# Kernel optimization log

Hardware: AMD Instinct MI355X
Metric: run time of the kernel (lower is better)

## Reference

```python
import jax, jax.numpy as jnp
import numpy as np

NUM_ITERS = 5
MIN_SCALE = 0.5
MAX_SCALE = 2.0
EPS = 1e-8


def setup_inputs() -> dict:
    key = jax.random.key(0)
    k1, k2 = jax.random.split(key)
    B, N, M = 16, 4096, 4096
    source = jax.random.normal(k1, (B, N, 3), dtype=jnp.float32)
    target = jax.random.normal(k2, (B, M, 3), dtype=jnp.float32)
    return {"source": source, "target": target}


def _sq_cdist(a, b):
    # squared euclidean distance matrix (B,N,M) via quadratic expansion
    a2 = jnp.sum(a * a, axis=-1)[:, :, None]
    b2 = jnp.sum(b * b, axis=-1)[:, None, :]
    ab = jnp.einsum('bnd,bmd->bnm', a, b)
    return jnp.maximum(a2 + b2 - 2.0 * ab, 0.0)


def _umeyama(source, target_corr):
    # optimal similarity transform (R, t, scale), Umeyama
    B = source.shape[0]
    mu_src = jnp.mean(source, axis=1, keepdims=True)       # (B,1,3)
    mu_tgt = jnp.mean(target_corr, axis=1, keepdims=True)  # (B,1,3)
    src_c = source - mu_src
    tgt_c = target_corr - mu_tgt
    H = jnp.einsum('bnd,bne->bde', src_c, tgt_c)           # (B,3,3)
    U, S, Vh = jnp.linalg.svd(H)
    V = jnp.swapaxes(Vh, 1, 2)
    det_UV = jnp.linalg.det(jnp.einsum('bij,bkj->bik', V, U))  # det(V U^T)
    d_diag = jnp.concatenate(
        [jnp.ones((B, 2), dtype=source.dtype), det_UV[:, None]], axis=1)  # (B,3)
    # R = V @ diag(d) @ U^T
    R = jnp.einsum('bij,bj,bkj->bik', V, d_diag, U)
    var_src = jnp.sum(src_c * src_c, axis=(1, 2))          # (B,)
    trace_S = jnp.sum(S * d_diag, axis=1)                  # (B,)
    scale = (trace_S / (var_src + EPS))[:, None, None]
    scale = jnp.clip(scale, MIN_SCALE, MAX_SCALE)
    t = mu_tgt - scale * jnp.einsum('bnd,bed->bne', mu_src, R)
    return R, t, scale


def reference(source, target):
    # ICP iterations (no-grad in original -> stop_gradient on final transform)
    src_current = source
    for _ in range(NUM_ITERS):
        dist = _sq_cdist(src_current, target)              # (B,N,M)
        min_idx = jnp.argmin(dist, axis=2)                 # (B,N)
        tgt_corr = jnp.take_along_axis(target, min_idx[:, :, None], axis=1)
        R, t, scale = _umeyama(source, tgt_corr)
        src_current = scale * jnp.einsum('bnd,bed->bne', source, R) + t
    R = jax.lax.stop_gradient(R)
    t = jax.lax.stop_gradient(t)
    scale = jax.lax.stop_gradient(scale)
    aligned_source = scale * jnp.einsum('bnd,bed->bne', source, R) + t
    final_dist = _sq_cdist(aligned_source, target)
    min_src2tgt = jnp.min(final_dist, axis=2)
    min_tgt2src = jnp.min(final_dist, axis=1)
    chamfer = jnp.mean(min_src2tgt, axis=1) + jnp.mean(min_tgt2src, axis=1)
    return jnp.mean(chamfer), aligned_source
```

## Files before the change

kernel.cpp:

```cpp
#include <hip/hip_runtime.h>
#include <math.h>

#define BLOCK 256
#define NB    16
#define NN_   4096
#define MM_   4096
#define NITER 5
#define P     4
#define SCH   4
#define KCH   16
#define TCH   256
#define KCHF  8
#define TCHF  512

#define OFF_STATS 0
#define OFF_T     64
#define OFF_CH    320
#define OFF_PART  336
#define OFF_ND    1280
#define OFF_FA    1280
#define OFF_FB    525568

typedef __attribute__((ext_vector_type(2))) float f32x2;

__device__ __forceinline__ f32x2 pk_fma(f32x2 a, f32x2 b, f32x2 c) {
  f32x2 d;
  asm("v_pk_fma_f32 %0, %1, %2, %3" : "=v"(d) : "v"(a), "v"(b), "v"(c));
  return d;
}

__global__ __launch_bounds__(BLOCK) void icp_init(const float* __restrict__ src,
                                                  float* __restrict__ ws) {
  int b = blockIdx.x, tid = threadIdx.x;
  const float* sb = src + (size_t)b * NN_ * 3;
  float sx = 0.f, sy = 0.f, sz = 0.f, ss = 0.f;
  for (int n = tid; n < NN_; n += BLOCK) {
    float x = sb[3*n], y = sb[3*n+1], z = sb[3*n+2];
    sx += x; sy += y; sz += z;
    ss += fmaf(x, x, fmaf(y, y, z*z));
  }
  __shared__ float red[16];
  for (int m = 32; m; m >>= 1) {
    sx += __shfl_xor(sx, m); sy += __shfl_xor(sy, m);
    sz += __shfl_xor(sz, m); ss += __shfl_xor(ss, m);
  }
  int wave = tid >> 6;
  if ((tid & 63) == 0) {
    red[wave*4+0] = sx; red[wave*4+1] = sy; red[wave*4+2] = sz; red[wave*4+3] = ss;
  }
  __syncthreads();
  if (tid == 0) {
    for (int w = 1; w < 4; ++w) {
      sx += red[w*4+0]; sy += red[w*4+1]; sz += red[w*4+2]; ss += red[w*4+3];
    }
    float* st = ws + OFF_STATS + b*4;
    st[0] = sx; st[1] = sy; st[2] = sz; st[3] = ss;
    float* T = ws + OFF_T + b*16;
    T[0]=1.f; T[1]=0.f; T[2]=0.f;
    T[3]=0.f; T[4]=1.f; T[5]=0.f;
    T[6]=0.f; T[7]=0.f; T[8]=1.f;
    T[9]=0.f; T[10]=0.f; T[11]=0.f; T[12]=1.f;
  }
}

__global__ __launch_bounds__(BLOCK) void icp_nn1(const float* __restrict__ src,
                                                 const float* __restrict__ tgt,
                                                 float* __restrict__ ws) {
  __shared__ float tx_[TCH], ty_[TCH], tz_[TCH], tw_[TCH];
  int b = blockIdx.z, kc = blockIdx.y, tid = threadIdx.x;
  int n0 = blockIdx.x * (BLOCK * P) + tid;
  const float* T = ws + OFF_T + b*16;
  float sc = T[12];
  f32x2 nxp[P], nyp[P], nzp[P];
#pragma unroll
  for (int k = 0; k < P; ++k) {
    const float* sp = src + ((size_t)b * NN_ + n0 + k*BLOCK) * 3;
    float sx = sp[0], sy = sp[1], sz = sp[2];
    float px = fmaf(sc, fmaf(T[0], sx, fmaf(T[1], sy, T[2]*sz)), T[9]);
    float py = fmaf(sc, fmaf(T[3], sx, fmaf(T[4], sy, T[5]*sz)), T[10]);
    float pz = fmaf(sc, fmaf(T[6], sx, fmaf(T[7], sy, T[8]*sz)), T[11]);
    nxp[k].x = nxp[k].y = -2.f*px;
    nyp[k].x = nyp[k].y = -2.f*py;
    nzp[k].x = nzp[k].y = -2.f*pz;
  }
  {
    int j = tid;
    const float* tp = tgt + ((size_t)b * MM_ + kc * TCH + j) * 3;
    float tx = tp[0], ty = tp[1], tz = tp[2];
    tx_[j] = tx; ty_[j] = ty; tz_[j] = tz;
    tw_[j] = fmaf(tx, tx, fmaf(ty, ty, tz*tz));
  }
  __syncthreads();

  int jbase = kc * TCH;
  float best[P];
#pragma unroll
  for (int k = 0; k < P; ++k) best[k] = INFINITY;
#pragma unroll 4
  for (int j = 0; j < TCH; j += 2) {
    f32x2 TX = *(const f32x2*)&tx_[j];
    f32x2 TY = *(const f32x2*)&ty_[j];
    f32x2 TZ = *(const f32x2*)&tz_[j];
    f32x2 TW = *(const f32x2*)&tw_[j];
#pragma unroll
    for (int k = 0; k < P; ++k) {
      f32x2 v = pk_fma(nxp[k], TX, pk_fma(nyp[k], TY, pk_fma(nzp[k], TZ, TW)));
      float p0 = __uint_as_float((__float_as_uint(v.x) & 0xFFFFF000u) |
                                 ((unsigned)(jbase + j) & 0xFFFu));
      float p1 = __uint_as_float((__float_as_uint(v.y) & 0xFFFFF000u) |
                                 ((unsigned)(jbase + j + 1) & 0xFFFu));
      best[k] = fminf(fminf(p0, p1), best[k]);
    }
  }
#pragma unroll
  for (int k = 0; k < P; ++k)
    ws[OFF_ND + (size_t)(b*KCH + kc)*NN_ + n0 + k*BLOCK] = best[k];
}

__global__ __launch_bounds__(BLOCK) void icp_nn2(const float* __restrict__ src,
                                                 const float* __restrict__ tgt,
                                                 float* __restrict__ ws) {
  __shared__ float red[4*12];
  int b = blockIdx.y, c4 = blockIdx.x, tid = threadIdx.x;
  float acc[12];
#pragma unroll
  for (int c = 0; c < 12; ++c) acc[c] = 0.f;
  for (int k = 0; k < P; ++k) {
    int n = c4 * (BLOCK*P) + tid + k*BLOCK;
    float bd = INFINITY;
#pragma unroll
    for (int c = 0; c < KCH; ++c)
      bd = fminf(bd, ws[OFF_ND + (size_t)(b*KCH + c)*NN_ + n]);
    int bi = (int)(__float_as_uint(bd) & 4095u);
    const float* tp = tgt + ((size_t)b * MM_ + bi) * 3;
    const float* sp = src + ((size_t)b * NN_ + n) * 3;
    float tx = tp[0], ty = tp[1], tz = tp[2];
    float sx = sp[0], sy = sp[1], sz = sp[2];
    acc[0] += tx; acc[1] += ty; acc[2] += tz;
    acc[3] += sx*tx; acc[4] += sx*ty; acc[5] += sx*tz;
    acc[6] += sy*tx; acc[7] += sy*ty; acc[8] += sy*tz;
    acc[9] += sz*tx; acc[10] += sz*ty; acc[11] += sz*tz;
  }
#pragma unroll
  for (int c = 0; c < 12; ++c)
    for (int m = 32; m; m >>= 1) acc[c] += __shfl_xor(acc[c], m);
  int wave = tid >> 6;
  if ((tid & 63) == 0) {
#pragma unroll
    for (int c = 0; c < 12; ++c) red[wave*12 + c] = acc[c];
  }
  __syncthreads();
  if (tid < 12) {
    float s = red[tid] + red[12+tid] + red[24+tid] + red[36+tid];
    ws[OFF_PART + (b*SCH + c4)*12 + tid] = s;
  }
}

__global__ __launch_bounds__(64) void icp_umeyama(float* __restrict__ ws) {
  int b = blockIdx.x, tid = threadIdx.x;
  __shared__ double sums[12];
  if (tid < 12) {
    double s = 0.0;
    for (int j = 0; j < SCH; ++j)
      s += (double)ws[OFF_PART + (b*SCH + j)*12 + tid];
    sums[tid] = s;
  }
  __syncthreads();
  if (tid != 0) return;

  const float* st = ws + OFF_STATS + b*4;
  const double N = (double)NN_;
  double mus[3] = {st[0]/N, st[1]/N, st[2]/N};
  double var_src = (double)st[3] - N*(mus[0]*mus[0] + mus[1]*mus[1] + mus[2]*mus[2]);
  double mut[3] = {sums[0]/N, sums[1]/N, sums[2]/N};
  double H[3][3];
  for (int d = 0; d < 3; ++d)
    for (int e = 0; e < 3; ++e)
      H[d][e] = sums[3 + 3*d + e] - N*mus[d]*mut[e];

  double A[3][3];
  for (int i = 0; i < 3; ++i)
    for (int j = 0; j < 3; ++j)
      A[i][j] = H[0][i]*H[0][j] + H[1][i]*H[1][j] + H[2][i]*H[2][j];
  double V[3][3] = {{1,0,0},{0,1,0},{0,0,1}};
  const int PP[3] = {0,0,1}, QQ[3] = {1,2,2};
  for (int sweep = 0; sweep < 14; ++sweep) {
    for (int r = 0; r < 3; ++r) {
      int p = PP[r], q = QQ[r];
      double apq = A[p][q];
      if (fabs(apq) < 1e-300) continue;
      double tau = (A[q][q] - A[p][p]) / (2.0*apq);
      double tt = (tau >= 0.0 ? 1.0 : -1.0) / (fabs(tau) + sqrt(1.0 + tau*tau));
      double c = 1.0 / sqrt(1.0 + tt*tt), s = tt*c;
      for (int k = 0; k < 3; ++k) { double akp=A[k][p], akq=A[k][q];
        A[k][p]=c*akp - s*akq; A[k][q]=s*akp + c*akq; }
      for (int k = 0; k < 3; ++k) { double apk=A[p][k], aqk=A[q][k];
        A[p][k]=c*apk - s*aqk; A[q][k]=s*apk + c*aqk; }
      for (int k = 0; k < 3; ++k) { double vkp=V[k][p], vkq=V[k][q];
        V[k][p]=c*vkp - s*vkq; V[k][q]=s*vkp + c*vkq; }
    }
  }
  double lam[3] = {A[0][0], A[1][1], A[2][2]};
  int o[3] = {0,1,2};
  if (lam[o[1]] > lam[o[0]]) { int t_=o[0]; o[0]=o[1]; o[1]=t_; }
  if (lam[o[2]] > lam[o[0]]) { int t_=o[0]; o[0]=o[2]; o[2]=t_; }
  if (lam[o[2]] > lam[o[1]]) { int t_=o[1]; o[1]=o[2]; o[2]=t_; }
  double v0[3] = {V[0][o[0]], V[1][o[0]], V[2][o[0]]};
  double v1[3] = {V[0][o[1]], V[1][o[1]], V[2][o[1]]};
  double v2[3] = {V[0][o[2]], V[1][o[2]], V[2][o[2]]};

  double hv0[3], hv1[3], hv2[3];
  for (int d = 0; d < 3; ++d) {
    hv0[d] = H[d][0]*v0[0] + H[d][1]*v0[1] + H[d][2]*v0[2];
    hv1[d] = H[d][0]*v1[0] + H[d][1]*v1[1] + H[d][2]*v1[2];
    hv2[d] = H[d][0]*v2[0] + H[d][1]*v2[1] + H[d][2]*v2[2];
  }
  double S0 = sqrt(hv0[0]*hv0[0] + hv0[1]*hv0[1] + hv0[2]*hv0[2]);
  double u0[3];
  double inv0 = (S0 > 1e-30) ? 1.0/S0 : 0.0;
  u0[0]=hv0[0]*inv0; u0[1]=hv0[1]*inv0; u0[2]=hv0[2]*inv0;
  if (S0 <= 1e-30) { u0[0]=1.0; u0[1]=0.0; u0[2]=0.0; }
  double S1 = sqrt(hv1[0]*hv1[0] + hv1[1]*hv1[1] + hv1[2]*hv1[2]);
  double d01 = u0[0]*hv1[0] + u0[1]*hv1[1] + u0[2]*hv1[2];
  double w1[3] = {hv1[0]-d01*u0[0], hv1[1]-d01*u0[1], hv1[2]-d01*u0[2]};
  double n1 = sqrt(w1[0]*w1[0] + w1[1]*w1[1] + w1[2]*w1[2]);
  double u1[3];
  if (n1 > 1e-30) { u1[0]=w1[0]/n1; u1[1]=w1[1]/n1; u1[2]=w1[2]/n1; }
  else {
    double ax = fabs(u0[0]);
    double t0[3] = { ax < 0.9 ? 1.0 : 0.0, ax < 0.9 ? 0.0 : 1.0, 0.0 };
    u1[0] = u0[1]*t0[2]-u0[2]*t0[1];
    u1[1] = u0[2]*t0[0]-u0[0]*t0[2];
    u1[2] = u0[0]*t0[1]-u0[1]*t0[0];
    double nn = sqrt(u1[0]*u1[0]+u1[1]*u1[1]+u1[2]*u1[2]);
    u1[0]/=nn; u1[1]/=nn; u1[2]/=nn;
  }
  double u2[3] = {u0[1]*u1[2]-u0[2]*u1[1],
                  u0[2]*u1[0]-u0[0]*u1[2],
                  u0[0]*u1[1]-u0[1]*u1[0]};
  double s2p = u2[0]*hv2[0] + u2[1]*hv2[1] + u2[2]*hv2[2];
  double dV = v0[0]*(v1[1]*v2[2]-v1[2]*v2[1])
            - v0[1]*(v1[0]*v2[2]-v1[2]*v2[0])
            + v0[2]*(v1[0]*v2[1]-v1[1]*v2[0]);
  dV = (dV >= 0.0) ? 1.0 : -1.0;
  double traceS = S0 + S1 + dV * s2p;

  double R[3][3];
  for (int i = 0; i < 3; ++i)
    for (int k = 0; k < 3; ++k)
      R[i][k] = v0[i]*u0[k] + v1[i]*u1[k] + dV*v2[i]*u2[k];

  double scale = traceS / (var_src + 1e-8);
  scale = fmin(fmax(scale, 0.5), 2.0);
  double tv[3];
  for (int e = 0; e < 3; ++e)
    tv[e] = mut[e] - scale*(R[e][0]*mus[0] + R[e][1]*mus[1] + R[e][2]*mus[2]);

  float* T = ws + OFF_T + b*16;
  for (int e = 0; e < 3; ++e)
    for (int d = 0; d < 3; ++d)
      T[3*e + d] = (float)R[e][d];
  T[9]  = (float)tv[0]; T[10] = (float)tv[1]; T[11] = (float)tv[2];
  T[12] = (float)scale;
}

__global__ __launch_bounds__(BLOCK) void icp_final(const float* __restrict__ src,
                                                   const float* __restrict__ tgt,
                                                   float* __restrict__ out,
                                                   float* __restrict__ ws) {
  __shared__ float tx_[TCHF], ty_[TCHF], tz_[TCHF], tw_[TCHF];
  int b = blockIdx.z, yk = blockIdx.y, tid = threadIdx.x;
  int dir = yk >> 3, kc = yk & 7;
  const float* T = ws + OFF_T + b*16;
  float sc = T[12];
  int n0 = blockIdx.x * (BLOCK * P) + tid;
  f32x2 nxp[P], nyp[P], nzp[P];
  float pp[P];

  if (dir == 0) {
#pragma unroll
    for (int k = 0; k < P; ++k) {
      const float* sp = src + ((size_t)b * NN_ + n0 + k*BLOCK) * 3;
      float sx = sp[0], sy = sp[1], sz = sp[2];
      float px = fmaf(sc, fmaf(T[0], sx, fmaf(T[1], sy, T[2]*sz)), T[9]);
      float py = fmaf(sc, fmaf(T[3], sx, fmaf(T[4], sy, T[5]*sz)), T[10]);
      float pz = fmaf(sc, fmaf(T[6], sx, fmaf(T[7], sy, T[8]*sz)), T[11]);
      if (kc == 0) {
        float* op = out + 1 + ((size_t)b * NN_ + n0 + k*BLOCK) * 3;
        op[0] = px; op[1] = py; op[2] = pz;
      }
      pp[k] = fmaf(px, px, fmaf(py, py, pz*pz));
      nxp[k].x = nxp[k].y = -2.f*px;
      nyp[k].x = nyp[k].y = -2.f*py;
      nzp[k].x = nzp[k].y = -2.f*pz;
    }
    const float* tb = tgt + ((size_t)b * MM_ + kc * TCHF) * 3;
    for (int j = tid; j < TCHF; j += BLOCK) {
      float tx = tb[3*j], ty = tb[3*j+1], tz = tb[3*j+2];
      tx_[j] = tx; ty_[j] = ty; tz_[j] = tz;
      tw_[j] = fmaf(tx, tx, fmaf(ty, ty, tz*tz));
    }
  } else {
#pragma unroll
    for (int k = 0; k < P; ++k) {
      const float* qp = tgt + ((size_t)b * MM_ + n0 + k*BLOCK) * 3;
      float qx = qp[0], qy = qp[1], qz = qp[2];
      pp[k] = fmaf(qx, qx, fmaf(qy, qy, qz*qz));
      nxp[k].x = nxp[k].y = -2.f*qx;
      nyp[k].x = nyp[k].y = -2.f*qy;
      nzp[k].x = nzp[k].y = -2.f*qz;
    }
    const float* sb = src + ((size_t)b * NN_ + kc * TCHF) * 3;
    for (int j = tid; j < TCHF; j += BLOCK) {
      float sx = sb[3*j], sy = sb[3*j+1], sz = sb[3*j+2];
      float ax = fmaf(sc, fmaf(T[0], sx, fmaf(T[1], sy, T[2]*sz)), T[9]);
      float ay = fmaf(sc, fmaf(T[3], sx, fmaf(T[4], sy, T[5]*sz)), T[10]);
      float az = fmaf(sc, fmaf(T[6], sx, fmaf(T[7], sy, T[8]*sz)), T[11]);
      tx_[j] = ax; ty_[j] = ay; tz_[j] = az;
      tw_[j] = fmaf(ax, ax, fmaf(ay, ay, az*az));
    }
  }
  __syncthreads();

  float best[P];
#pragma unroll
  for (int k = 0; k < P; ++k) best[k] = INFINITY;
#pragma unroll 4
  for (int j = 0; j < TCHF; j += 2) {
    f32x2 TX = *(const f32x2*)&tx_[j];
    f32x2 TY = *(const f32x2*)&ty_[j];
    f32x2 TZ = *(const f32x2*)&tz_[j];
    f32x2 TW = *(const f32x2*)&tw_[j];
#pragma unroll
    for (int k = 0; k < P; ++k) {
      f32x2 v = pk_fma(nxp[k], TX, pk_fma(nyp[k], TY, pk_fma(nzp[k], TZ, TW)));
      best[k] = fminf(fminf(v.x, v.y), best[k]);
    }
  }
  float* dst = ws + (dir ? OFF_FB : OFF_FA);
#pragma unroll
  for (int k = 0; k < P; ++k)
    dst[(size_t)(b*KCHF + kc)*NN_ + n0 + k*BLOCK] = best[k] + pp[k];
}

__global__ __launch_bounds__(BLOCK) void icp_fcomb(float* __restrict__ ws) {
  __shared__ float red[4*2];
  int b = blockIdx.x, tid = threadIdx.x;
  float sa = 0.f, sb = 0.f;
  for (int g = 0; g < NN_/BLOCK; ++g) {
    int n = g*BLOCK + tid;
    float m1 = INFINITY, m2 = INFINITY;
#pragma unroll
    for (int c = 0; c < KCHF; ++c) {
      m1 = fminf(m1, ws[OFF_FA + (size_t)(b*KCHF + c)*NN_ + n]);
      m2 = fminf(m2, ws[OFF_FB + (size_t)(b*KCHF + c)*MM_ + n]);
    }
    sa += fmaxf(m1, 0.f);
    sb += fmaxf(m2, 0.f);
  }
  for (int m = 32; m; m >>= 1) {
    sa += __shfl_xor(sa, m); sb += __shfl_xor(sb, m);
  }
  int wave = tid >> 6;
  if ((tid & 63) == 0) { red[wave*2] = sa; red[wave*2+1] = sb; }
  __syncthreads();
  if (tid == 0) {
    sa = red[0] + red[2] + red[4] + red[6];
    sb = red[1] + red[3] + red[5] + red[7];
    ws[OFF_CH + b] = sa / (float)NN_ + sb / (float)MM_;
  }
}

__global__ __launch_bounds__(64) void icp_finalize(float* __restrict__ out,
                                                   const float* __restrict__ ws) {
  if (threadIdx.x == 0) {
    float s = 0.f;
    for (int b = 0; b < NB; ++b) s += ws[OFF_CH + b];
    out[0] = s / (float)NB;
  }
}

extern "C" void kernel_launch(void* const* d_in, const int* in_sizes, int n_in,
                              void* d_out, int out_size, void* d_ws, size_t ws_size,
                              hipStream_t stream) {
  const float* src = (const float*)d_in[0];
  const float* tgt = (const float*)d_in[1];
  float* out = (float*)d_out;
  float* ws  = (float*)d_ws;

  icp_init<<<NB, BLOCK, 0, stream>>>(src, ws);
  for (int it = 0; it < NITER; ++it) {
    icp_nn1<<<dim3(SCH, KCH, NB), BLOCK, 0, stream>>>(src, tgt, ws);
    icp_nn2<<<dim3(SCH, NB), BLOCK, 0, stream>>>(src, tgt, ws);
    icp_umeyama<<<NB, 64, 0, stream>>>(ws);
  }
  icp_final<<<dim3(SCH, 2*KCHF, NB), BLOCK, 0, stream>>>(src, tgt, out, ws);
  icp_fcomb<<<NB, BLOCK, 0, stream>>>(ws);
  icp_finalize<<<1, 64, 0, stream>>>(out, ws);
}
```

Before: 356.7 us.

## Reduce nearest-neighbour partials with float atomicMin and use finer target chunks

Per-chunk nearest-neighbour partial buffers are replaced by a single per-point slot updated with unsigned atomicMin on the float bits. The slots are cleared to infinity in init and reset in nn2 after reading. This removes the KCH-wide combine loops in nn2 and fcomb. Target chunks are halved to launch more blocks, occupancy hints are added, and Jacobi sweeps drop from 14 to 8. In exchange the inner loop adds |p|^2 to every packed distance so values stay non-negative for the integer compare. That costs an extra packed add per pair, and any tiny negative rounding result would break the min ordering.

```diff
diff --git a/kernel.cpp b/kernel.cpp
--- a/kernel.cpp
+++ b/kernel.cpp
@@ -8,18 +8,22 @@
 #define NITER 5
 #define P     4
 #define SCH   4
-#define KCH   16
-#define TCH   256
-#define KCHF  8
-#define TCHF  512
+#define KCH   32
+#define TCH   128
+#define KCHF  16
+#define TCHF  256
+#define SCH2  4
+#define P2    4
 
 #define OFF_STATS 0
 #define OFF_T     64
 #define OFF_CH    320
 #define OFF_PART  336
-#define OFF_ND    1280
-#define OFF_FA    1280
-#define OFF_FB    525568
+#define OFF_ND    2048
+#define OFF_FA    67584
+#define OFF_FB    133120
+#define CLR_BASE  2048
+#define CLR_CNT   196608
 
 typedef __attribute__((ext_vector_type(2))) float f32x2;
 
@@ -29,9 +33,15 @@
   return d;
 }
 
+__device__ __forceinline__ void atomic_min_f(float* p, float v) {
+  atomicMin((unsigned int*)p, __float_as_uint(v));
+}
+
 __global__ __launch_bounds__(BLOCK) void icp_init(const float* __restrict__ src,
                                                   float* __restrict__ ws) {
   int b = blockIdx.x, tid = threadIdx.x;
+  for (int i = b*BLOCK + tid; i < CLR_CNT; i += NB*BLOCK)
+    ws[CLR_BASE + i] = INFINITY;
   const float* sb = src + (size_t)b * NN_ * 3;
   float sx = 0.f, sy = 0.f, sz = 0.f, ss = 0.f;
   for (int n = tid; n < NN_; n += BLOCK) {
@@ -63,15 +73,15 @@
   }
 }
 
-__global__ __launch_bounds__(BLOCK) void icp_nn1(const float* __restrict__ src,
-                                                 const float* __restrict__ tgt,
-                                                 float* __restrict__ ws) {
-  __shared__ float tx_[TCH], ty_[TCH], tz_[TCH], tw_[TCH];
+__global__ __launch_bounds__(BLOCK, 8) void icp_nn1(const float* __restrict__ src,
+                                                    const float* __restrict__ tgt,
+                                                    float* __restrict__ ws) {
+  __shared__ __align__(16) float tx_[TCH], ty_[TCH], tz_[TCH], tw_[TCH];
   int b = blockIdx.z, kc = blockIdx.y, tid = threadIdx.x;
   int n0 = blockIdx.x * (BLOCK * P) + tid;
   const float* T = ws + OFF_T + b*16;
   float sc = T[12];
-  f32x2 nxp[P], nyp[P], nzp[P];
+  f32x2 nxp[P], nyp[P], nzp[P], p2p[P];
 #pragma unroll
   for (int k = 0; k < P; ++k) {
     const float* sp = src + ((size_t)b * NN_ + n0 + k*BLOCK) * 3;
@@ -82,8 +92,10 @@
     nxp[k].x = nxp[k].y = -2.f*px;
     nyp[k].x = nyp[k].y = -2.f*py;
     nzp[k].x = nzp[k].y = -2.f*pz;
-  }
-  {
+    float p2 = fmaf(px, px, fmaf(py, py, pz*pz));
+    p2p[k].x = p2p[k].y = p2;
+  }
+  if (tid < TCH) {
     int j = tid;
     const float* tp = tgt + ((size_t)b * MM_ + kc * TCH + j) * 3;
     float tx = tp[0], ty = tp[1], tz = tp[2];
@@ -102,19 +114,18 @@
     f32x2 TY = *(const f32x2*)&ty_[j];
     f32x2 TZ = *(const f32x2*)&tz_[j];
     f32x2 TW = *(const f32x2*)&tw_[j];
+    unsigned i0 = (unsigned)(jbase + j), i1 = i0 + 1;
 #pragma unroll
     for (int k = 0; k < P; ++k) {
-      f32x2 v = pk_fma(nxp[k], TX, pk_fma(nyp[k], TY, pk_fma(nzp[k], TZ, TW)));
-      float p0 = __uint_as_float((__float_as_uint(v.x) & 0xFFFFF000u) |
-                                 ((unsigned)(jbase + j) & 0xFFFu));
-      float p1 = __uint_as_float((__float_as_uint(v.y) & 0xFFFFF000u) |
-                                 ((unsigned)(jbase + j + 1) & 0xFFFu));
+      f32x2 v = pk_fma(nxp[k], TX, pk_fma(nyp[k], TY, pk_fma(nzp[k], TZ, TW + p2p[k])));
+      float p0 = __uint_as_float((__float_as_uint(v.x) & 0xFFFFF000u) | i0);
+      float p1 = __uint_as_float((__float_as_uint(v.y) & 0xFFFFF000u) | i1);
       best[k] = fminf(fminf(p0, p1), best[k]);
     }
   }
 #pragma unroll
   for (int k = 0; k < P; ++k)
-    ws[OFF_ND + (size_t)(b*KCH + kc)*NN_ + n0 + k*BLOCK] = best[k];
+    atomic_min_f(ws + OFF_ND + (size_t)b*NN_ + n0 + k*BLOCK, best[k]);
 }
 
 __global__ __launch_bounds__(BLOCK) void icp_nn2(const float* __restrict__ src,
@@ -125,12 +136,11 @@
   float acc[12];
 #pragma unroll
   for (int c = 0; c < 12; ++c) acc[c] = 0.f;
-  for (int k = 0; k < P; ++k) {
-    int n = c4 * (BLOCK*P) + tid + k*BLOCK;
-    float bd = INFINITY;
-#pragma unroll
-    for (int c = 0; c < KCH; ++c)
-      bd = fminf(bd, ws[OFF_ND + (size_t)(b*KCH + c)*NN_ + n]);
+  for (int k = 0; k < P2; ++k) {
+    int n = c4 * (BLOCK*P2) + tid + k*BLOCK;
+    size_t slot = OFF_ND + (size_t)b*NN_ + n;
+    float bd = ws[slot];
+    ws[slot] = INFINITY;
     int bi = (int)(__float_as_uint(bd) & 4095u);
     const float* tp = tgt + ((size_t)b * MM_ + bi) * 3;
     const float* sp = src + ((size_t)b * NN_ + n) * 3;
@@ -152,7 +162,7 @@
   __syncthreads();
   if (tid < 12) {
     float s = red[tid] + red[12+tid] + red[24+tid] + red[36+tid];
-    ws[OFF_PART + (b*SCH + c4)*12 + tid] = s;
+    ws[OFF_PART + (b*SCH2 + c4)*12 + tid] = s;
   }
 }
 
@@ -161,8 +171,8 @@
   __shared__ double sums[12];
   if (tid < 12) {
     double s = 0.0;
-    for (int j = 0; j < SCH; ++j)
-      s += (double)ws[OFF_PART + (b*SCH + j)*12 + tid];
+    for (int j = 0; j < SCH2; ++j)
+      s += (double)ws[OFF_PART + (b*SCH2 + j)*12 + tid];
     sums[tid] = s;
   }
   __syncthreads();
@@ -184,7 +194,7 @@
       A[i][j] = H[0][i]*H[0][j] + H[1][i]*H[1][j] + H[2][i]*H[2][j];
   double V[3][3] = {{1,0,0},{0,1,0},{0,0,1}};
   const int PP[3] = {0,0,1}, QQ[3] = {1,2,2};
-  for (int sweep = 0; sweep < 14; ++sweep) {
+  for (int sweep = 0; sweep < 8; ++sweep) {
     for (int r = 0; r < 3; ++r) {
       int p = PP[r], q = QQ[r];
       double apq = A[p][q];
@@ -264,13 +274,13 @@
   T[12] = (float)scale;
 }
 
-__global__ __launch_bounds__(BLOCK) void icp_final(const float* __restrict__ src,
-                                                   const float* __restrict__ tgt,
-                                                   float* __restrict__ out,
-                                                   float* __restrict__ ws) {
-  __shared__ float tx_[TCHF], ty_[TCHF], tz_[TCHF], tw_[TCHF];
+__global__ __launch_bounds__(BLOCK, 8) void icp_final(const float* __restrict__ src,
+                                                      const float* __restrict__ tgt,
+                                                      float* __restrict__ out,
+                                                      float* __restrict__ ws) {
+  __shared__ __align__(16) float tx_[TCHF], ty_[TCHF], tz_[TCHF], tw_[TCHF];
   int b = blockIdx.z, yk = blockIdx.y, tid = threadIdx.x;
-  int dir = yk >> 3, kc = yk & 7;
+  int dir = yk >> 4, kc = yk & 15;
   const float* T = ws + OFF_T + b*16;
   float sc = T[12];
   int n0 = blockIdx.x * (BLOCK * P) + tid;
@@ -295,7 +305,8 @@
       nzp[k].x = nzp[k].y = -2.f*pz;
     }
     const float* tb = tgt + ((size_t)b * MM_ + kc * TCHF) * 3;
-    for (int j = tid; j < TCHF; j += BLOCK) {
+    {
+      int j = tid;
       float tx = tb[3*j], ty = tb[3*j+1], tz = tb[3*j+2];
       tx_[j] = tx; ty_[j] = ty; tz_[j] = tz;
       tw_[j] = fmaf(tx, tx, fmaf(ty, ty, tz*tz));
@@ -311,7 +322,8 @@
       nzp[k].x = nzp[k].y = -2.f*qz;
     }
     const float* sb = src + ((size_t)b * NN_ + kc * TCHF) * 3;
-    for (int j = tid; j < TCHF; j += BLOCK) {
+    {
+      int j = tid;
       float sx = sb[3*j], sy = sb[3*j+1], sz = sb[3*j+2];
       float ax = fmaf(sc, fmaf(T[0], sx, fmaf(T[1], sy, T[2]*sz)), T[9]);
       float ay = fmaf(sc, fmaf(T[3], sx, fmaf(T[4], sy, T[5]*sz)), T[10]);
@@ -339,8 +351,10 @@
   }
   float* dst = ws + (dir ? OFF_FB : OFF_FA);
 #pragma unroll
-  for (int k = 0; k < P; ++k)
-    dst[(size_t)(b*KCHF + kc)*NN_ + n0 + k*BLOCK] = best[k] + pp[k];
+  for (int k = 0; k < P; ++k) {
+    float v = fmaxf(best[k] + pp[k], 0.f);
+    atomic_min_f(dst + (size_t)b*NN_ + n0 + k*BLOCK, v);
+  }
 }
 
 __global__ __launch_bounds__(BLOCK) void icp_fcomb(float* __restrict__ ws) {
@@ -349,14 +363,8 @@
   float sa = 0.f, sb = 0.f;
   for (int g = 0; g < NN_/BLOCK; ++g) {
     int n = g*BLOCK + tid;
-    float m1 = INFINITY, m2 = INFINITY;
-#pragma unroll
-    for (int c = 0; c < KCHF; ++c) {
-      m1 = fminf(m1, ws[OFF_FA + (size_t)(b*KCHF + c)*NN_ + n]);
-      m2 = fminf(m2, ws[OFF_FB + (size_t)(b*KCHF + c)*MM_ + n]);
-    }
-    sa += fmaxf(m1, 0.f);
-    sb += fmaxf(m2, 0.f);
+    sa += ws[OFF_FA + (size_t)b*NN_ + n];
+    sb += ws[OFF_FB + (size_t)b*NN_ + n];
   }
   for (int m = 32; m; m >>= 1) {
     sa += __shfl_xor(sa, m); sb += __shfl_xor(sb, m);
@@ -391,7 +399,7 @@
   icp_init<<<NB, BLOCK, 0, stream>>>(src, ws);
   for (int it = 0; it < NITER; ++it) {
     icp_nn1<<<dim3(SCH, KCH, NB), BLOCK, 0, stream>>>(src, tgt, ws);
-    icp_nn2<<<dim3(SCH, NB), BLOCK, 0, stream>>>(src, tgt, ws);
+    icp_nn2<<<dim3(SCH2, NB), BLOCK, 0, stream>>>(src, tgt, ws);
     icp_umeyama<<<NB, 64, 0, stream>>>(ws);
   }
   icp_final<<<dim3(SCH, 2*KCHF, NB), BLOCK, 0, stream>>>(src, tgt, out, ws);
```

New measurement: 322.6 us. 1.11x faster.
